# Optimization experiments

Hardware: AMD Instinct MI355X
Metric: run time of the kernel (lower is better)

Reference implementation:

```python
import jax, jax.numpy as jnp
import numpy as np

B, L, C, OUT = 8, 256, 512, 512


def setup_inputs() -> dict:
    key = jax.random.key(0)
    ks = jax.random.split(key, 8)
    xd = jax.random.normal(ks[0], (B, L, C), jnp.float32)
    xt = jax.random.normal(ks[1], (B, L, C), jnp.float32)
    # Linear weights stored (in, out): y = x @ W + b (equiv. to torch x @ W^T)
    Wc = jax.random.normal(ks[2], (C, C), jnp.float32) * 0.02
    bc = jnp.zeros((C,), jnp.float32)
    Wp = jax.random.normal(ks[3], (C, C), jnp.float32) * 0.02
    bp = jnp.zeros((C,), jnp.float32)
    Wf = jax.random.normal(ks[4], (C, OUT), jnp.float32) * 0.02
    bf = jnp.zeros((OUT,), jnp.float32)
    return {"xd": xd, "xt": xt, "Wc": Wc, "bc": bc, "Wp": Wp, "bp": bp, "Wf": Wf, "bf": bf}


def reference(xd, xt, Wc, bc, Wp, bp, Wf, bf):
    # projected features
    pt = jax.nn.relu(xt) @ Wp + bp              # (b, Lt, C)
    pc = jax.nn.relu(xd) @ Wc + bc              # (b, Ld, C)
    # sigmoid bilinear scores: (b, Lt, Ld) == (b, Ld, Lt) since Lt == Ld structurally
    scores = jax.nn.sigmoid(jnp.einsum('bic,bkc->bik', pt, pc))
    # normalize by total per-batch sum
    w = scores / jnp.sum(scores, axis=(1, 2), keepdims=True)
    # tanh of elementwise outer product, reduced with attention weights
    # cp[b,c] = sum_{i,j} tanh(xd[b,i,c] * xt[b,j,c]) * w[b,i,j]
    cp = jnp.einsum('bijc,bij->bc', jnp.tanh(xd[:, :, None, :] * xt[:, None, :, :]), w)
    return cp @ Wf + bf
```

## Files before the change

kernel.cpp:

```cpp
#include <hip/hip_runtime.h>
#include <math.h>

#define B_   8
#define L_   256
#define C_   512
#define OUT_ 512

typedef _Float16 half8 __attribute__((ext_vector_type(8)));
typedef _Float16 half4 __attribute__((ext_vector_type(4)));
typedef float    f32x4 __attribute__((ext_vector_type(4)));
typedef float    f32x2 __attribute__((ext_vector_type(2)));

__global__ __launch_bounds__(256)
void proj_mfma_kernel(const float* __restrict__ xt, const float* __restrict__ Wp,
                      const float* __restrict__ bp,
                      const float* __restrict__ xd, const float* __restrict__ Wc,
                      const float* __restrict__ bc,
                      _Float16* __restrict__ pt, _Float16* __restrict__ pc)
{
    const int which = blockIdx.z;
    const float* __restrict__ X    = which ? xd : xt;
    const float* __restrict__ W    = which ? Wc : Wp;
    const float* __restrict__ bias = which ? bc : bp;
    _Float16*    __restrict__ Y    = which ? pc : pt;

    __shared__ _Float16 Ah[2][64][40];
    __shared__ _Float16 Bh[2][64][40];
    __shared__ _Float16 Ot[64][72];

    const int tid = threadIdx.x;
    const int m0 = blockIdx.y << 6, n0 = blockIdx.x << 6;
    const int lane = tid & 63, wv = tid >> 6;
    const int l15 = lane & 15, quad = lane >> 4;

    const int srow = tid >> 2, sch = (tid & 3) << 3;
    const float* Ag = X + (size_t)(m0 + srow) * C_ + sch;
    const int nl = tid & 63, kseg = tid >> 6;
    const float* Bg = W + (size_t)(kseg << 3) * C_ + n0 + nl;

    float4 a0 = *(const float4*)(Ag);
    float4 a1 = *(const float4*)(Ag + 4);
    float wr[8];
    #pragma unroll
    for (int r = 0; r < 8; ++r) wr[r] = Bg[(size_t)r * C_];

    {
        half8 av;
        av[0] = (_Float16)fmaxf(a0.x, 0.f); av[1] = (_Float16)fmaxf(a0.y, 0.f);
        av[2] = (_Float16)fmaxf(a0.z, 0.f); av[3] = (_Float16)fmaxf(a0.w, 0.f);
        av[4] = (_Float16)fmaxf(a1.x, 0.f); av[5] = (_Float16)fmaxf(a1.y, 0.f);
        av[6] = (_Float16)fmaxf(a1.z, 0.f); av[7] = (_Float16)fmaxf(a1.w, 0.f);
        *(half8*)&Ah[0][srow][sch] = av;
        half8 bv;
        #pragma unroll
        for (int r = 0; r < 8; ++r) bv[r] = (_Float16)wr[r];
        *(half8*)&Bh[0][nl][kseg << 3] = bv;
    }

    f32x4 acc[4] = {};
    for (int ks = 0; ks < 16; ++ks) {
        const int cur = ks & 1;
        if (ks < 15) {
            Ag += 32;
            Bg += 32 * C_;
            a0 = *(const float4*)(Ag);
            a1 = *(const float4*)(Ag + 4);
            #pragma unroll
            for (int r = 0; r < 8; ++r) wr[r] = Bg[(size_t)r * C_];
        }
        __syncthreads();
        half8 af = *(const half8*)&Ah[cur][(wv << 4) + l15][quad << 3];
        #pragma unroll
        for (int nb = 0; nb < 4; ++nb) {
            half8 bf = *(const half8*)&Bh[cur][(nb << 4) + l15][quad << 3];
            acc[nb] = __builtin_amdgcn_mfma_f32_16x16x32_f16(af, bf, acc[nb], 0, 0, 0);
        }
        if (ks < 15) {
            half8 av;
            av[0] = (_Float16)fmaxf(a0.x, 0.f); av[1] = (_Float16)fmaxf(a0.y, 0.f);
            av[2] = (_Float16)fmaxf(a0.z, 0.f); av[3] = (_Float16)fmaxf(a0.w, 0.f);
            av[4] = (_Float16)fmaxf(a1.x, 0.f); av[5] = (_Float16)fmaxf(a1.y, 0.f);
            av[6] = (_Float16)fmaxf(a1.z, 0.f); av[7] = (_Float16)fmaxf(a1.w, 0.f);
            *(half8*)&Ah[cur ^ 1][srow][sch] = av;
            half8 bv;
            #pragma unroll
            for (int r = 0; r < 8; ++r) bv[r] = (_Float16)wr[r];
            *(half8*)&Bh[cur ^ 1][nl][kseg << 3] = bv;
        }
    }

    __syncthreads();
    #pragma unroll
    for (int nb = 0; nb < 4; ++nb) {
        const float bz = bias[n0 + (nb << 4) + l15];
        #pragma unroll
        for (int r = 0; r < 4; ++r)
            Ot[(wv << 4) + (quad << 2) + r][(nb << 4) + l15] = (_Float16)(acc[nb][r] + bz);
    }
    __syncthreads();
    const int erow = tid >> 3, ech = (tid & 7) << 3;
    #pragma unroll
    for (int h = 0; h < 64; h += 32)
        *(half8*)&Y[(size_t)(m0 + erow + h) * C_ + n0 + ech] = *(const half8*)&Ot[erow + h][ech];
}

__device__ __forceinline__ float sigmoid_fast(float z) {
    float e = __builtin_amdgcn_exp2f(-1.4426950408889634f * z);
    return __builtin_amdgcn_rcpf(e + 1.0f);
}

__global__ __launch_bounds__(256)
void scores_kernel(const _Float16* __restrict__ pt, const _Float16* __restrict__ pc,
                   float* __restrict__ w, float* __restrict__ sums_part)
{
    const int bx = blockIdx.x, by = blockIdx.y, b = blockIdx.z;
    const int i0 = bx << 5, j0 = by << 5;
    const int tid = threadIdx.x;
    const int lane = tid & 63, wv = tid >> 6;
    const int l15 = lane & 15, quad = lane >> 4;
    const int mq = wv >> 1, nq = wv & 1;

    __shared__ float wred[4];

    const _Float16* __restrict__ Ap =
        pt + (size_t)(b * L_ + i0 + mq * 16 + l15) * C_ + (quad << 3);
    const _Float16* __restrict__ Bp =
        pc + (size_t)(b * L_ + j0 + nq * 16 + l15) * C_ + (quad << 3);

    f32x4 acc = {};
    #pragma unroll
    for (int ks = 0; ks < 16; ++ks) {
        half8 af = *(const half8*)(Ap + (ks << 5));
        half8 bf = *(const half8*)(Bp + (ks << 5));
        acc = __builtin_amdgcn_mfma_f32_16x16x32_f16(af, bf, acc, 0, 0, 0);
    }

    float4 sg;
    sg.x = sigmoid_fast(acc[0]);
    sg.y = sigmoid_fast(acc[1]);
    sg.z = sigmoid_fast(acc[2]);
    sg.w = sigmoid_fast(acc[3]);

    float* __restrict__ wp =
        w + (size_t)(b * L_ + i0 + mq * 16 + (quad << 2)) * L_ + j0 + nq * 16 + l15;
    wp[0 * L_] = sg.x;
    wp[1 * L_] = sg.y;
    wp[2 * L_] = sg.z;
    wp[3 * L_] = sg.w;

    float lsum = (sg.x + sg.y) + (sg.z + sg.w);
    #pragma unroll
    for (int off = 32; off; off >>= 1) lsum += __shfl_xor(lsum, off);
    if (lane == 0) wred[wv] = lsum;
    __syncthreads();
    if (tid == 0)
        sums_part[(b << 6) | (bx << 3) | by] = (wred[0] + wred[1]) + (wred[2] + wred[3]);
}

__global__ __launch_bounds__(512, 8)
void tanh_cp_kernel(const float* __restrict__ w, const float* __restrict__ xd,
                    const float* __restrict__ xt, float* __restrict__ partials)
{
    const int bx = blockIdx.x, by = blockIdx.y, b = blockIdx.z;
    const int i0 = bx << 4, j0 = by << 4;
    const int tid = threadIdx.x;

    __shared__ float ws_[16][20];

    if (tid < 64) {
        const int ir = tid >> 2, j4 = (tid & 3) << 2;
        const float4 v = *(const float4*)(w + (size_t)(b * L_ + i0 + ir) * L_ + j0 + j4);
        ws_[j4 + 0][ir] = v.x;
        ws_[j4 + 1][ir] = v.y;
        ws_[j4 + 2][ir] = v.z;
        ws_[j4 + 3][ir] = v.w;
    }

    const int c = tid;
    const float* __restrict__ xdb = xd + (size_t)(b * L_ + i0) * C_ + c;
    const float* __restrict__ xtb = xt + (size_t)(b * L_ + j0) * C_ + c;

    f32x2 xds2[8];
    #pragma unroll
    for (int i = 0; i < 8; ++i) {
        xds2[i].x = xdb[(size_t)(2 * i) * C_];
        xds2[i].y = xdb[(size_t)(2 * i + 1) * C_];
    }

    __syncthreads();

    f32x2 acc01 = {0.f, 0.f}, acc23 = {0.f, 0.f};
    #pragma unroll
    for (int jj = 0; jj < 16; ++jj) {
        const float xv = xtb[(size_t)jj * C_] * 2.8853900817779268f;
        #pragma unroll
        for (int i = 0; i < 16; i += 4) {
            const float4 w4 = *(const float4*)&ws_[jj][i];
            f32x2 x01 = xds2[i >> 1] * xv;
            f32x2 e01 = { __builtin_amdgcn_exp2f(x01.x), __builtin_amdgcn_exp2f(x01.y) };
            f32x2 q01 = e01 + 1.0f;
            float rp01 = __builtin_amdgcn_rcpf(q01.x * q01.y);
            f32x2 r01 = rp01 * __builtin_shufflevector(q01, q01, 1, 0);
            f32x2 w01 = { w4.x, w4.y };
            acc01 = w01 * r01 + acc01;
            f32x2 x23 = xds2[(i >> 1) + 1] * xv;
            f32x2 e23 = { __builtin_amdgcn_exp2f(x23.x), __builtin_amdgcn_exp2f(x23.y) };
            f32x2 q23 = e23 + 1.0f;
            float rp23 = __builtin_amdgcn_rcpf(q23.x * q23.y);
            f32x2 r23 = rp23 * __builtin_shufflevector(q23, q23, 1, 0);
            f32x2 w23 = { w4.z, w4.w };
            acc23 = w23 * r23 + acc23;
        }
    }
    const int p = (bx << 4) | by;
    partials[(size_t)((b << 8) | p) * C_ + c] =
        (acc01.x + acc01.y) + (acc23.x + acc23.y);
}

__global__ __launch_bounds__(512)
void finalize_kernel(const float* __restrict__ partials, const float* __restrict__ sums_part,
                     const float* __restrict__ Wf, const float* __restrict__ bfv,
                     float* __restrict__ out)
{
    const int b = blockIdx.y;
    const int t = threadIdx.x;
    __shared__ float cp[C_];
    __shared__ float red[512];
    __shared__ float sumsh;

    red[t] = (t < 64) ? sums_part[(b << 6) | t] : 0.f;

    float s = 0.f;
    #pragma unroll 8
    for (int p = 0; p < 256; ++p)
        s += partials[(size_t)((b << 8) | p) * C_ + t];

    __syncthreads();
    for (int st = 256; st > 0; st >>= 1) {
        if (t < st) red[t] += red[t + st];
        __syncthreads();
    }
    if (t == 0) sumsh = red[0];
    __syncthreads();

    cp[t] = 1.0f - 2.0f * s / sumsh;
    __syncthreads();

    const int o  = ((int)blockIdx.x << 6) | (t & 63);
    const int c0 = (t >> 6) << 6;
    float acc = 0.f;
    #pragma unroll 8
    for (int i = 0; i < 64; ++i) {
        const int cc = c0 + i;
        acc = fmaf(cp[cc], Wf[(size_t)cc * OUT_ + o], acc);
    }
    red[t] = acc;
    __syncthreads();
    if (t < 64) {
        float a = 0.f;
        #pragma unroll
        for (int g = 0; g < 8; ++g) a += red[(g << 6) | t];
        out[(size_t)b * OUT_ + o] = a + bfv[o];
    }
}

extern "C" void kernel_launch(void* const* d_in, const int* in_sizes, int n_in,
                              void* d_out, int out_size, void* d_ws, size_t ws_size,
                              hipStream_t stream)
{
    const float* xd = (const float*)d_in[0];
    const float* xt = (const float*)d_in[1];
    const float* Wc = (const float*)d_in[2];
    const float* bc = (const float*)d_in[3];
    const float* Wp = (const float*)d_in[4];
    const float* bp = (const float*)d_in[5];
    const float* Wf = (const float*)d_in[6];
    const float* bf = (const float*)d_in[7];
    float* out = (float*)d_out;

    _Float16* pt = (_Float16*)d_ws;
    _Float16* pc = pt + 1048576;
    float* w         = (float*)(pc + 1048576);
    float* partials  = w + 524288;
    float* sums_part = partials + 1048576;

    proj_mfma_kernel<<<dim3(8, 32, 2), 256, 0, stream>>>(xt, Wp, bp, xd, Wc, bc, pt, pc);
    scores_kernel<<<dim3(8, 8, 8), 256, 0, stream>>>(pt, pc, w, sums_part);
    tanh_cp_kernel<<<dim3(16, 16, 8), 512, 0, stream>>>(w, xd, xt, partials);
    finalize_kernel<<<dim3(8, 8), 512, 0, stream>>>(partials, sums_part, Wf, bf, out);
}
```

Before: 151.6 us.

## Add fp16 prep pass, restructure projection and scores GEMMs, pipeline tanh loop

Adds a prep kernel that converts relu(x) to fp16 and transposes the weights to fp16, so the projection GEMM can read MFMA fragments straight from global memory with no LDS staging. The projection and scores kernels now give each wave one 16x16 tile with two independent accumulator chains, and the score tiles are re-shaped. The tanh kernel preloads all xt values into registers, software-pipelines its LDS weight reads across a flattened loop, changes the LDS padding and lowers the occupancy hint. This costs one extra launch and an extra global round trip for the converted data, and raises register pressure in the tanh kernel.

```diff
diff --git a/kernel.cpp b/kernel.cpp
--- a/kernel.cpp
+++ b/kernel.cpp
@@ -12,96 +12,92 @@
 typedef float    f32x2 __attribute__((ext_vector_type(2)));
 
 __global__ __launch_bounds__(256)
-void proj_mfma_kernel(const float* __restrict__ xt, const float* __restrict__ Wp,
-                      const float* __restrict__ bp,
-                      const float* __restrict__ xd, const float* __restrict__ Wc,
-                      const float* __restrict__ bc,
-                      _Float16* __restrict__ pt, _Float16* __restrict__ pc)
-{
-    const int which = blockIdx.z;
-    const float* __restrict__ X    = which ? xd : xt;
-    const float* __restrict__ W    = which ? Wc : Wp;
-    const float* __restrict__ bias = which ? bc : bp;
-    _Float16*    __restrict__ Y    = which ? pc : pt;
-
-    __shared__ _Float16 Ah[2][64][40];
-    __shared__ _Float16 Bh[2][64][40];
-    __shared__ _Float16 Ot[64][72];
-
+void prep_kernel(const float* __restrict__ xt, const float* __restrict__ xd,
+                 const float* __restrict__ Wp, const float* __restrict__ Wc,
+                 _Float16* __restrict__ Xth, _Float16* __restrict__ Xdh,
+                 _Float16* __restrict__ Wpt, _Float16* __restrict__ Wct)
+{
+    const int task = blockIdx.z;
     const int tid = threadIdx.x;
-    const int m0 = blockIdx.y << 6, n0 = blockIdx.x << 6;
-    const int lane = tid & 63, wv = tid >> 6;
-    const int l15 = lane & 15, quad = lane >> 4;
-
-    const int srow = tid >> 2, sch = (tid & 3) << 3;
-    const float* Ag = X + (size_t)(m0 + srow) * C_ + sch;
-    const int nl = tid & 63, kseg = tid >> 6;
-    const float* Bg = W + (size_t)(kseg << 3) * C_ + n0 + nl;
-
-    float4 a0 = *(const float4*)(Ag);
-    float4 a1 = *(const float4*)(Ag + 4);
-    float wr[8];
-    #pragma unroll
-    for (int r = 0; r < 8; ++r) wr[r] = Bg[(size_t)r * C_];
-
-    {
-        half8 av;
-        av[0] = (_Float16)fmaxf(a0.x, 0.f); av[1] = (_Float16)fmaxf(a0.y, 0.f);
-        av[2] = (_Float16)fmaxf(a0.z, 0.f); av[3] = (_Float16)fmaxf(a0.w, 0.f);
-        av[4] = (_Float16)fmaxf(a1.x, 0.f); av[5] = (_Float16)fmaxf(a1.y, 0.f);
-        av[6] = (_Float16)fmaxf(a1.z, 0.f); av[7] = (_Float16)fmaxf(a1.w, 0.f);
-        *(half8*)&Ah[0][srow][sch] = av;
-        half8 bv;
-        #pragma unroll
-        for (int r = 0; r < 8; ++r) bv[r] = (_Float16)wr[r];
-        *(half8*)&Bh[0][nl][kseg << 3] = bv;
-    }
-
-    f32x4 acc[4] = {};
-    for (int ks = 0; ks < 16; ++ks) {
-        const int cur = ks & 1;
-        if (ks < 15) {
-            Ag += 32;
-            Bg += 32 * C_;
-            a0 = *(const float4*)(Ag);
-            a1 = *(const float4*)(Ag + 4);
-            #pragma unroll
-            for (int r = 0; r < 8; ++r) wr[r] = Bg[(size_t)r * C_];
+    if (task < 2) {
+        const float* __restrict__ src = task ? xd : xt;
+        _Float16*    __restrict__ dst = task ? Xdh : Xth;
+        const size_t base = (size_t)blockIdx.x * 16384;
+        #pragma unroll
+        for (int it = 0; it < 16; ++it) {
+            const size_t o = base + ((size_t)it * 256 + tid) * 4;
+            const float4 v = *(const float4*)(src + o);
+            half4 h;
+            h[0] = (_Float16)fmaxf(v.x, 0.f);
+            h[1] = (_Float16)fmaxf(v.y, 0.f);
+            h[2] = (_Float16)fmaxf(v.z, 0.f);
+            h[3] = (_Float16)fmaxf(v.w, 0.f);
+            *(half4*)(dst + o) = h;
+        }
+    } else {
+        const float* __restrict__ src = (task == 3) ? Wc : Wp;
+        _Float16*    __restrict__ dst = (task == 3) ? Wct : Wpt;
+        __shared__ _Float16 tr[64][80];
+        const int tx = (blockIdx.x & 7) << 6;
+        const int ty = (blockIdx.x >> 3) << 6;
+        const int r0 = tid >> 4;
+        const int c4 = (tid & 15) << 2;
+        #pragma unroll
+        for (int p = 0; p < 4; ++p) {
+            const int kr = r0 + (p << 4);
+            const float4 v = *(const float4*)(src + (size_t)(tx + kr) * C_ + ty + c4);
+            tr[c4 + 0][kr] = (_Float16)v.x;
+            tr[c4 + 1][kr] = (_Float16)v.y;
+            tr[c4 + 2][kr] = (_Float16)v.z;
+            tr[c4 + 3][kr] = (_Float16)v.w;
         }
         __syncthreads();
-        half8 af = *(const half8*)&Ah[cur][(wv << 4) + l15][quad << 3];
-        #pragma unroll
-        for (int nb = 0; nb < 4; ++nb) {
-            half8 bf = *(const half8*)&Bh[cur][(nb << 4) + l15][quad << 3];
-            acc[nb] = __builtin_amdgcn_mfma_f32_16x16x32_f16(af, bf, acc[nb], 0, 0, 0);
-        }
-        if (ks < 15) {
-            half8 av;
-            av[0] = (_Float16)fmaxf(a0.x, 0.f); av[1] = (_Float16)fmaxf(a0.y, 0.f);
-            av[2] = (_Float16)fmaxf(a0.z, 0.f); av[3] = (_Float16)fmaxf(a0.w, 0.f);
-            av[4] = (_Float16)fmaxf(a1.x, 0.f); av[5] = (_Float16)fmaxf(a1.y, 0.f);
-            av[6] = (_Float16)fmaxf(a1.z, 0.f); av[7] = (_Float16)fmaxf(a1.w, 0.f);
-            *(half8*)&Ah[cur ^ 1][srow][sch] = av;
-            half8 bv;
-            #pragma unroll
-            for (int r = 0; r < 8; ++r) bv[r] = (_Float16)wr[r];
-            *(half8*)&Bh[cur ^ 1][nl][kseg << 3] = bv;
-        }
-    }
-
-    __syncthreads();
-    #pragma unroll
-    for (int nb = 0; nb < 4; ++nb) {
-        const float bz = bias[n0 + (nb << 4) + l15];
-        #pragma unroll
-        for (int r = 0; r < 4; ++r)
-            Ot[(wv << 4) + (quad << 2) + r][(nb << 4) + l15] = (_Float16)(acc[nb][r] + bz);
-    }
-    __syncthreads();
-    const int erow = tid >> 3, ech = (tid & 7) << 3;
-    #pragma unroll
-    for (int h = 0; h < 64; h += 32)
-        *(half8*)&Y[(size_t)(m0 + erow + h) * C_ + n0 + ech] = *(const half8*)&Ot[erow + h][ech];
+        const int nr = tid >> 3;
+        const int k8 = (tid & 7) << 3;
+        #pragma unroll
+        for (int p = 0; p < 2; ++p)
+            *(half8*)(dst + (size_t)(ty + nr + (p << 5)) * C_ + tx + k8) =
+                *(const half8*)&tr[nr + (p << 5)][k8];
+    }
+}
+
+__global__ __launch_bounds__(512)
+void proj_mfma_kernel(const _Float16* __restrict__ Xth, const _Float16* __restrict__ Xdh,
+                      const _Float16* __restrict__ Wpt, const _Float16* __restrict__ Wct,
+                      const float* __restrict__ bp, const float* __restrict__ bc,
+                      _Float16* __restrict__ pt, _Float16* __restrict__ pc)
+{
+    const int which = blockIdx.y;
+    const _Float16* __restrict__ Xh = which ? Xdh : Xth;
+    const _Float16* __restrict__ Wt = which ? Wct : Wpt;
+    const float*    __restrict__ bias = which ? bc : bp;
+    _Float16*       __restrict__ Y  = which ? pc : pt;
+
+    const int tid = threadIdx.x;
+    const int wv = tid >> 6, lane = tid & 63;
+    const int l15 = lane & 15, quad = lane >> 4;
+    const int id = ((int)blockIdx.x << 3) + wv;
+    const int m0 = (id >> 5) << 4;
+    const int n0 = (id & 31) << 4;
+
+    const _Float16* __restrict__ Ap = Xh + (size_t)(m0 + l15) * C_ + (quad << 3);
+    const _Float16* __restrict__ Bp = Wt + (size_t)(n0 + l15) * C_ + (quad << 3);
+
+    f32x4 acc0 = {}, acc1 = {};
+    #pragma unroll
+    for (int ks = 0; ks < 8; ++ks) {
+        half8 a0 = *(const half8*)(Ap + (ks << 5));
+        half8 b0 = *(const half8*)(Bp + (ks << 5));
+        acc0 = __builtin_amdgcn_mfma_f32_16x16x32_f16(a0, b0, acc0, 0, 0, 0);
+        half8 a1 = *(const half8*)(Ap + ((ks + 8) << 5));
+        half8 b1 = *(const half8*)(Bp + ((ks + 8) << 5));
+        acc1 = __builtin_amdgcn_mfma_f32_16x16x32_f16(a1, b1, acc1, 0, 0, 0);
+    }
+    const f32x4 acc = acc0 + acc1;
+    const float bz = bias[n0 + l15];
+    #pragma unroll
+    for (int r = 0; r < 4; ++r)
+        Y[(size_t)(m0 + (quad << 2) + r) * C_ + n0 + l15] = (_Float16)(acc[r] + bz);
 }
 
 __device__ __forceinline__ float sigmoid_fast(float z) {
@@ -109,31 +105,33 @@
     return __builtin_amdgcn_rcpf(e + 1.0f);
 }
 
-__global__ __launch_bounds__(256)
+__global__ __launch_bounds__(512)
 void scores_kernel(const _Float16* __restrict__ pt, const _Float16* __restrict__ pc,
                    float* __restrict__ w, float* __restrict__ sums_part)
 {
     const int bx = blockIdx.x, by = blockIdx.y, b = blockIdx.z;
-    const int i0 = bx << 5, j0 = by << 5;
     const int tid = threadIdx.x;
-    const int lane = tid & 63, wv = tid >> 6;
+    const int wv = tid >> 6, lane = tid & 63;
     const int l15 = lane & 15, quad = lane >> 4;
-    const int mq = wv >> 1, nq = wv & 1;
-
-    __shared__ float wred[4];
-
-    const _Float16* __restrict__ Ap =
-        pt + (size_t)(b * L_ + i0 + mq * 16 + l15) * C_ + (quad << 3);
-    const _Float16* __restrict__ Bp =
-        pc + (size_t)(b * L_ + j0 + nq * 16 + l15) * C_ + (quad << 3);
-
-    f32x4 acc = {};
-    #pragma unroll
-    for (int ks = 0; ks < 16; ++ks) {
-        half8 af = *(const half8*)(Ap + (ks << 5));
-        half8 bf = *(const half8*)(Bp + (ks << 5));
-        acc = __builtin_amdgcn_mfma_f32_16x16x32_f16(af, bf, acc, 0, 0, 0);
-    }
+    const int i0 = ((bx << 3) + wv) << 4;
+    const int j0 = by << 4;
+
+    __shared__ float wred[8];
+
+    const _Float16* __restrict__ Ap = pt + (size_t)(b * L_ + i0 + l15) * C_ + (quad << 3);
+    const _Float16* __restrict__ Bp = pc + (size_t)(b * L_ + j0 + l15) * C_ + (quad << 3);
+
+    f32x4 acc0 = {}, acc1 = {};
+    #pragma unroll
+    for (int ks = 0; ks < 8; ++ks) {
+        half8 a0 = *(const half8*)(Ap + (ks << 5));
+        half8 b0 = *(const half8*)(Bp + (ks << 5));
+        acc0 = __builtin_amdgcn_mfma_f32_16x16x32_f16(a0, b0, acc0, 0, 0, 0);
+        half8 a1 = *(const half8*)(Ap + ((ks + 8) << 5));
+        half8 b1 = *(const half8*)(Bp + ((ks + 8) << 5));
+        acc1 = __builtin_amdgcn_mfma_f32_16x16x32_f16(a1, b1, acc1, 0, 0, 0);
+    }
+    const f32x4 acc = acc0 + acc1;
 
     float4 sg;
     sg.x = sigmoid_fast(acc[0]);
@@ -141,8 +139,7 @@
     sg.z = sigmoid_fast(acc[2]);
     sg.w = sigmoid_fast(acc[3]);
 
-    float* __restrict__ wp =
-        w + (size_t)(b * L_ + i0 + mq * 16 + (quad << 2)) * L_ + j0 + nq * 16 + l15;
+    float* __restrict__ wp = w + (size_t)(b * L_ + i0 + (quad << 2)) * L_ + j0 + l15;
     wp[0 * L_] = sg.x;
     wp[1 * L_] = sg.y;
     wp[2 * L_] = sg.z;
@@ -153,11 +150,15 @@
     for (int off = 32; off; off >>= 1) lsum += __shfl_xor(lsum, off);
     if (lane == 0) wred[wv] = lsum;
     __syncthreads();
-    if (tid == 0)
-        sums_part[(b << 6) | (bx << 3) | by] = (wred[0] + wred[1]) + (wred[2] + wred[3]);
-}
-
-__global__ __launch_bounds__(512, 8)
+    if (tid == 0) {
+        float s = 0.f;
+        #pragma unroll
+        for (int v = 0; v < 8; ++v) s += wred[v];
+        sums_part[(b << 5) | (by << 1) | bx] = s;
+    }
+}
+
+__global__ __launch_bounds__(512, 6)
 void tanh_cp_kernel(const float* __restrict__ w, const float* __restrict__ xd,
                     const float* __restrict__ xt, float* __restrict__ partials)
 {
@@ -165,7 +166,7 @@
     const int i0 = bx << 4, j0 = by << 4;
     const int tid = threadIdx.x;
 
-    __shared__ float ws_[16][20];
+    __shared__ float ws_[16][24];
 
     if (tid < 64) {
         const int ir = tid >> 2, j4 = (tid & 3) << 2;
@@ -180,6 +181,11 @@
     const float* __restrict__ xdb = xd + (size_t)(b * L_ + i0) * C_ + c;
     const float* __restrict__ xtb = xt + (size_t)(b * L_ + j0) * C_ + c;
 
+    float xtv[16];
+    #pragma unroll
+    for (int j = 0; j < 16; ++j)
+        xtv[j] = xtb[(size_t)j * C_] * 2.8853900817779268f;
+
     f32x2 xds2[8];
     #pragma unroll
     for (int i = 0; i < 8; ++i) {
@@ -190,27 +196,32 @@
     __syncthreads();
 
     f32x2 acc01 = {0.f, 0.f}, acc23 = {0.f, 0.f};
-    #pragma unroll
-    for (int jj = 0; jj < 16; ++jj) {
-        const float xv = xtb[(size_t)jj * C_] * 2.8853900817779268f;
-        #pragma unroll
-        for (int i = 0; i < 16; i += 4) {
-            const float4 w4 = *(const float4*)&ws_[jj][i];
-            f32x2 x01 = xds2[i >> 1] * xv;
-            f32x2 e01 = { __builtin_amdgcn_exp2f(x01.x), __builtin_amdgcn_exp2f(x01.y) };
-            f32x2 q01 = e01 + 1.0f;
-            float rp01 = __builtin_amdgcn_rcpf(q01.x * q01.y);
-            f32x2 r01 = rp01 * __builtin_shufflevector(q01, q01, 1, 0);
-            f32x2 w01 = { w4.x, w4.y };
-            acc01 = w01 * r01 + acc01;
-            f32x2 x23 = xds2[(i >> 1) + 1] * xv;
-            f32x2 e23 = { __builtin_amdgcn_exp2f(x23.x), __builtin_amdgcn_exp2f(x23.y) };
-            f32x2 q23 = e23 + 1.0f;
-            float rp23 = __builtin_amdgcn_rcpf(q23.x * q23.y);
-            f32x2 r23 = rp23 * __builtin_shufflevector(q23, q23, 1, 0);
-            f32x2 w23 = { w4.z, w4.w };
-            acc23 = w23 * r23 + acc23;
+    float4 wb0 = *(const float4*)&ws_[0][0];
+    float4 wb1 = *(const float4*)&ws_[0][4];
+    #pragma unroll
+    for (int q = 0; q < 64; ++q) {
+        float4 wn = wb1;
+        if (q < 62) {
+            const int qq = q + 2;
+            wn = *(const float4*)&ws_[qq >> 2][(qq & 3) << 2];
         }
+        const float xv = xtv[q >> 2];
+        const int h = (q & 3) << 1;
+        f32x2 x01 = xds2[h] * xv;
+        f32x2 e01 = { __builtin_amdgcn_exp2f(x01.x), __builtin_amdgcn_exp2f(x01.y) };
+        f32x2 q01 = e01 + 1.0f;
+        float rp01 = __builtin_amdgcn_rcpf(q01.x * q01.y);
+        f32x2 r01 = rp01 * __builtin_shufflevector(q01, q01, 1, 0);
+        f32x2 w01 = { wb0.x, wb0.y };
+        acc01 = w01 * r01 + acc01;
+        f32x2 x23 = xds2[h + 1] * xv;
+        f32x2 e23 = { __builtin_amdgcn_exp2f(x23.x), __builtin_amdgcn_exp2f(x23.y) };
+        f32x2 q23 = e23 + 1.0f;
+        float rp23 = __builtin_amdgcn_rcpf(q23.x * q23.y);
+        f32x2 r23 = rp23 * __builtin_shufflevector(q23, q23, 1, 0);
+        f32x2 w23 = { wb0.z, wb0.w };
+        acc23 = w23 * r23 + acc23;
+        wb0 = wb1; wb1 = wn;
     }
     const int p = (bx << 4) | by;
     partials[(size_t)((b << 8) | p) * C_ + c] =
@@ -228,7 +239,7 @@
     __shared__ float red[512];
     __shared__ float sumsh;
 
-    red[t] = (t < 64) ? sums_part[(b << 6) | t] : 0.f;
+    red[t] = (t < 32) ? sums_part[(b << 5) | t] : 0.f;
 
     float s = 0.f;
     #pragma unroll 8
@@ -278,14 +289,19 @@
     const float* bf = (const float*)d_in[7];
     float* out = (float*)d_out;
 
-    _Float16* pt = (_Float16*)d_ws;
-    _Float16* pc = pt + 1048576;
+    _Float16* Xth = (_Float16*)d_ws;
+    _Float16* Xdh = Xth + 1048576;
+    _Float16* Wpt = Xdh + 1048576;
+    _Float16* Wct = Wpt + 262144;
+    _Float16* pt  = Wct + 262144;
+    _Float16* pc  = pt + 1048576;
     float* w         = (float*)(pc + 1048576);
     float* partials  = w + 524288;
     float* sums_part = partials + 1048576;
 
-    proj_mfma_kernel<<<dim3(8, 32, 2), 256, 0, stream>>>(xt, Wp, bp, xd, Wc, bc, pt, pc);
-    scores_kernel<<<dim3(8, 8, 8), 256, 0, stream>>>(pt, pc, w, sums_part);
+    prep_kernel<<<dim3(64, 1, 4), 256, 0, stream>>>(xt, xd, Wp, Wc, Xth, Xdh, Wpt, Wct);
+    proj_mfma_kernel<<<dim3(512, 2), 512, 0, stream>>>(Xth, Xdh, Wpt, Wct, bp, bc, pt, pc);
+    scores_kernel<<<dim3(2, 16, 8), 512, 0, stream>>>(pt, pc, w, sums_part);
     tanh_cp_kernel<<<dim3(16, 16, 8), 512, 0, stream>>>(w, xd, xt, partials);
     finalize_kernel<<<dim3(8, 8), 512, 0, stream>>>(partials, sums_part, Wf, bf, out);
 }
```

Result: slower. 174.3 us (+15.0%).

## Fuse all stages into one persistent kernel with grid barriers

Applied to the files above, without the earlier changes.

Replaces the four launches with a single persistent 512-block kernel that uses atomic grid barriers between phases. The phases are fp16 relu pre-conversion plus a weight transpose, the projection GEMM, a fused scores-sigmoid-tanh reduction, and the finalize. Scores no longer round-trip through global memory, and launch gaps go away. In exchange it adds a memset plus barrier spin costs, and it relies on all 512 blocks being co-resident or the barrier deadlocks.

```diff
diff --git a/kernel.cpp b/kernel.cpp
--- a/kernel.cpp
+++ b/kernel.cpp
@@ -5,262 +5,245 @@
 #define L_   256
 #define C_   512
 #define OUT_ 512
+#define NB   512
+#define NT   512
 
 typedef _Float16 half8 __attribute__((ext_vector_type(8)));
 typedef _Float16 half4 __attribute__((ext_vector_type(4)));
 typedef float    f32x4 __attribute__((ext_vector_type(4)));
 typedef float    f32x2 __attribute__((ext_vector_type(2)));
 
-__global__ __launch_bounds__(256)
-void proj_mfma_kernel(const float* __restrict__ xt, const float* __restrict__ Wp,
-                      const float* __restrict__ bp,
-                      const float* __restrict__ xd, const float* __restrict__ Wc,
-                      const float* __restrict__ bc,
-                      _Float16* __restrict__ pt, _Float16* __restrict__ pc)
-{
-    const int which = blockIdx.z;
-    const float* __restrict__ X    = which ? xd : xt;
-    const float* __restrict__ W    = which ? Wc : Wp;
-    const float* __restrict__ bias = which ? bc : bp;
-    _Float16*    __restrict__ Y    = which ? pc : pt;
-
-    __shared__ _Float16 Ah[2][64][40];
-    __shared__ _Float16 Bh[2][64][40];
-    __shared__ _Float16 Ot[64][72];
-
-    const int tid = threadIdx.x;
-    const int m0 = blockIdx.y << 6, n0 = blockIdx.x << 6;
-    const int lane = tid & 63, wv = tid >> 6;
-    const int l15 = lane & 15, quad = lane >> 4;
-
-    const int srow = tid >> 2, sch = (tid & 3) << 3;
-    const float* Ag = X + (size_t)(m0 + srow) * C_ + sch;
-    const int nl = tid & 63, kseg = tid >> 6;
-    const float* Bg = W + (size_t)(kseg << 3) * C_ + n0 + nl;
-
-    float4 a0 = *(const float4*)(Ag);
-    float4 a1 = *(const float4*)(Ag + 4);
-    float wr[8];
-    #pragma unroll
-    for (int r = 0; r < 8; ++r) wr[r] = Bg[(size_t)r * C_];
-
-    {
-        half8 av;
-        av[0] = (_Float16)fmaxf(a0.x, 0.f); av[1] = (_Float16)fmaxf(a0.y, 0.f);
-        av[2] = (_Float16)fmaxf(a0.z, 0.f); av[3] = (_Float16)fmaxf(a0.w, 0.f);
-        av[4] = (_Float16)fmaxf(a1.x, 0.f); av[5] = (_Float16)fmaxf(a1.y, 0.f);
-        av[6] = (_Float16)fmaxf(a1.z, 0.f); av[7] = (_Float16)fmaxf(a1.w, 0.f);
-        *(half8*)&Ah[0][srow][sch] = av;
-        half8 bv;
-        #pragma unroll
-        for (int r = 0; r < 8; ++r) bv[r] = (_Float16)wr[r];
-        *(half8*)&Bh[0][nl][kseg << 3] = bv;
-    }
-
-    f32x4 acc[4] = {};
-    for (int ks = 0; ks < 16; ++ks) {
-        const int cur = ks & 1;
-        if (ks < 15) {
-            Ag += 32;
-            Bg += 32 * C_;
-            a0 = *(const float4*)(Ag);
-            a1 = *(const float4*)(Ag + 4);
-            #pragma unroll
-            for (int r = 0; r < 8; ++r) wr[r] = Bg[(size_t)r * C_];
-        }
-        __syncthreads();
-        half8 af = *(const half8*)&Ah[cur][(wv << 4) + l15][quad << 3];
-        #pragma unroll
-        for (int nb = 0; nb < 4; ++nb) {
-            half8 bf = *(const half8*)&Bh[cur][(nb << 4) + l15][quad << 3];
-            acc[nb] = __builtin_amdgcn_mfma_f32_16x16x32_f16(af, bf, acc[nb], 0, 0, 0);
-        }
-        if (ks < 15) {
-            half8 av;
-            av[0] = (_Float16)fmaxf(a0.x, 0.f); av[1] = (_Float16)fmaxf(a0.y, 0.f);
-            av[2] = (_Float16)fmaxf(a0.z, 0.f); av[3] = (_Float16)fmaxf(a0.w, 0.f);
-            av[4] = (_Float16)fmaxf(a1.x, 0.f); av[5] = (_Float16)fmaxf(a1.y, 0.f);
-            av[6] = (_Float16)fmaxf(a1.z, 0.f); av[7] = (_Float16)fmaxf(a1.w, 0.f);
-            *(half8*)&Ah[cur ^ 1][srow][sch] = av;
-            half8 bv;
-            #pragma unroll
-            for (int r = 0; r < 8; ++r) bv[r] = (_Float16)wr[r];
-            *(half8*)&Bh[cur ^ 1][nl][kseg << 3] = bv;
-        }
-    }
-
-    __syncthreads();
-    #pragma unroll
-    for (int nb = 0; nb < 4; ++nb) {
-        const float bz = bias[n0 + (nb << 4) + l15];
-        #pragma unroll
-        for (int r = 0; r < 4; ++r)
-            Ot[(wv << 4) + (quad << 2) + r][(nb << 4) + l15] = (_Float16)(acc[nb][r] + bz);
-    }
-    __syncthreads();
-    const int erow = tid >> 3, ech = (tid & 7) << 3;
-    #pragma unroll
-    for (int h = 0; h < 64; h += 32)
-        *(half8*)&Y[(size_t)(m0 + erow + h) * C_ + n0 + ech] = *(const half8*)&Ot[erow + h][ech];
-}
+
+struct SmemA { _Float16 tr[64][80]; };
+struct SmemC { float red[8][256]; float ws[2][16][20]; float wred[8]; };
+struct SmemD { float cp[C_]; float redf[NT]; };
+union __align__(16) SmemU { SmemA a; SmemC c; SmemD d; };
 
 __device__ __forceinline__ float sigmoid_fast(float z) {
     float e = __builtin_amdgcn_exp2f(-1.4426950408889634f * z);
     return __builtin_amdgcn_rcpf(e + 1.0f);
 }
 
-__global__ __launch_bounds__(256)
-void scores_kernel(const _Float16* __restrict__ pt, const _Float16* __restrict__ pc,
-                   float* __restrict__ w, float* __restrict__ sums_part)
+__device__ __forceinline__ void grid_barrier(unsigned* __restrict__ bar, int k) {
+    __syncthreads();
+    if (threadIdx.x == 0) {
+        __threadfence();
+        unsigned arrived = __hip_atomic_fetch_add(&bar[k], 1u, __ATOMIC_ACQ_REL,
+                                                  __HIP_MEMORY_SCOPE_AGENT) + 1u;
+        if (arrived < (unsigned)NB) {
+            while (__hip_atomic_load(&bar[k], __ATOMIC_ACQUIRE,
+                                     __HIP_MEMORY_SCOPE_AGENT) < (unsigned)NB)
+                __builtin_amdgcn_s_sleep(8);
+        }
+    }
+    __syncthreads();
+}
+
+__global__ __launch_bounds__(NT, 4)
+void mega_kernel(const float* __restrict__ xd, const float* __restrict__ xt,
+                 const float* __restrict__ Wc, const float* __restrict__ bc,
+                 const float* __restrict__ Wp, const float* __restrict__ bp,
+                 const float* __restrict__ Wf, const float* __restrict__ bfv,
+                 unsigned* __restrict__ bar,
+                 _Float16* __restrict__ Xth, _Float16* __restrict__ Xdh,
+                 _Float16* __restrict__ Wpt, _Float16* __restrict__ Wct,
+                 _Float16* __restrict__ pt, _Float16* __restrict__ pc,
+                 float* __restrict__ cpart, float* __restrict__ tile_sum,
+                 float* __restrict__ out)
 {
-    const int bx = blockIdx.x, by = blockIdx.y, b = blockIdx.z;
-    const int i0 = bx << 5, j0 = by << 5;
-    const int tid = threadIdx.x;
-    const int lane = tid & 63, wv = tid >> 6;
-    const int l15 = lane & 15, quad = lane >> 4;
-    const int mq = wv >> 1, nq = wv & 1;
-
-    __shared__ float wred[4];
-
-    const _Float16* __restrict__ Ap =
-        pt + (size_t)(b * L_ + i0 + mq * 16 + l15) * C_ + (quad << 3);
-    const _Float16* __restrict__ Bp =
-        pc + (size_t)(b * L_ + j0 + nq * 16 + l15) * C_ + (quad << 3);
-
-    f32x4 acc = {};
-    #pragma unroll
-    for (int ks = 0; ks < 16; ++ks) {
-        half8 af = *(const half8*)(Ap + (ks << 5));
-        half8 bf = *(const half8*)(Bp + (ks << 5));
-        acc = __builtin_amdgcn_mfma_f32_16x16x32_f16(af, bf, acc, 0, 0, 0);
-    }
-
-    float4 sg;
-    sg.x = sigmoid_fast(acc[0]);
-    sg.y = sigmoid_fast(acc[1]);
-    sg.z = sigmoid_fast(acc[2]);
-    sg.w = sigmoid_fast(acc[3]);
-
-    float* __restrict__ wp =
-        w + (size_t)(b * L_ + i0 + mq * 16 + (quad << 2)) * L_ + j0 + nq * 16 + l15;
-    wp[0 * L_] = sg.x;
-    wp[1 * L_] = sg.y;
-    wp[2 * L_] = sg.z;
-    wp[3 * L_] = sg.w;
-
-    float lsum = (sg.x + sg.y) + (sg.z + sg.w);
-    #pragma unroll
-    for (int off = 32; off; off >>= 1) lsum += __shfl_xor(lsum, off);
-    if (lane == 0) wred[wv] = lsum;
-    __syncthreads();
-    if (tid == 0)
-        sums_part[(b << 6) | (bx << 3) | by] = (wred[0] + wred[1]) + (wred[2] + wred[3]);
-}
-
-__global__ __launch_bounds__(512, 8)
-void tanh_cp_kernel(const float* __restrict__ w, const float* __restrict__ xd,
-                    const float* __restrict__ xt, float* __restrict__ partials)
-{
-    const int bx = blockIdx.x, by = blockIdx.y, b = blockIdx.z;
-    const int i0 = bx << 4, j0 = by << 4;
-    const int tid = threadIdx.x;
-
-    __shared__ float ws_[16][20];
-
-    if (tid < 64) {
-        const int ir = tid >> 2, j4 = (tid & 3) << 2;
-        const float4 v = *(const float4*)(w + (size_t)(b * L_ + i0 + ir) * L_ + j0 + j4);
-        ws_[j4 + 0][ir] = v.x;
-        ws_[j4 + 1][ir] = v.y;
-        ws_[j4 + 2][ir] = v.z;
-        ws_[j4 + 3][ir] = v.w;
-    }
-
-    const int c = tid;
-    const float* __restrict__ xdb = xd + (size_t)(b * L_ + i0) * C_ + c;
-    const float* __restrict__ xtb = xt + (size_t)(b * L_ + j0) * C_ + c;
-
-    f32x2 xds2[8];
-    #pragma unroll
-    for (int i = 0; i < 8; ++i) {
-        xds2[i].x = xdb[(size_t)(2 * i) * C_];
-        xds2[i].y = xdb[(size_t)(2 * i + 1) * C_];
-    }
-
-    __syncthreads();
-
-    f32x2 acc01 = {0.f, 0.f}, acc23 = {0.f, 0.f};
-    #pragma unroll
-    for (int jj = 0; jj < 16; ++jj) {
-        const float xv = xtb[(size_t)jj * C_] * 2.8853900817779268f;
-        #pragma unroll
-        for (int i = 0; i < 16; i += 4) {
-            const float4 w4 = *(const float4*)&ws_[jj][i];
-            f32x2 x01 = xds2[i >> 1] * xv;
-            f32x2 e01 = { __builtin_amdgcn_exp2f(x01.x), __builtin_amdgcn_exp2f(x01.y) };
-            f32x2 q01 = e01 + 1.0f;
-            float rp01 = __builtin_amdgcn_rcpf(q01.x * q01.y);
-            f32x2 r01 = rp01 * __builtin_shufflevector(q01, q01, 1, 0);
-            f32x2 w01 = { w4.x, w4.y };
-            acc01 = w01 * r01 + acc01;
-            f32x2 x23 = xds2[(i >> 1) + 1] * xv;
-            f32x2 e23 = { __builtin_amdgcn_exp2f(x23.x), __builtin_amdgcn_exp2f(x23.y) };
-            f32x2 q23 = e23 + 1.0f;
-            float rp23 = __builtin_amdgcn_rcpf(q23.x * q23.y);
-            f32x2 r23 = rp23 * __builtin_shufflevector(q23, q23, 1, 0);
-            f32x2 w23 = { w4.z, w4.w };
-            acc23 = w23 * r23 + acc23;
-        }
-    }
-    const int p = (bx << 4) | by;
-    partials[(size_t)((b << 8) | p) * C_ + c] =
-        (acc01.x + acc01.y) + (acc23.x + acc23.y);
-}
-
-__global__ __launch_bounds__(512)
-void finalize_kernel(const float* __restrict__ partials, const float* __restrict__ sums_part,
-                     const float* __restrict__ Wf, const float* __restrict__ bfv,
-                     float* __restrict__ out)
-{
-    const int b = blockIdx.y;
-    const int t = threadIdx.x;
-    __shared__ float cp[C_];
-    __shared__ float red[512];
-    __shared__ float sumsh;
-
-    red[t] = (t < 64) ? sums_part[(b << 6) | t] : 0.f;
-
-    float s = 0.f;
-    #pragma unroll 8
-    for (int p = 0; p < 256; ++p)
-        s += partials[(size_t)((b << 8) | p) * C_ + t];
-
-    __syncthreads();
-    for (int st = 256; st > 0; st >>= 1) {
-        if (t < st) red[t] += red[t + st];
-        __syncthreads();
-    }
-    if (t == 0) sumsh = red[0];
-    __syncthreads();
-
-    cp[t] = 1.0f - 2.0f * s / sumsh;
-    __syncthreads();
-
-    const int o  = ((int)blockIdx.x << 6) | (t & 63);
-    const int c0 = (t >> 6) << 6;
-    float acc = 0.f;
-    #pragma unroll 8
-    for (int i = 0; i < 64; ++i) {
-        const int cc = c0 + i;
-        acc = fmaf(cp[cc], Wf[(size_t)cc * OUT_ + o], acc);
-    }
-    red[t] = acc;
-    __syncthreads();
-    if (t < 64) {
-        float a = 0.f;
-        #pragma unroll
-        for (int g = 0; g < 8; ++g) a += red[(g << 6) | t];
-        out[(size_t)b * OUT_ + o] = a + bfv[o];
+    __shared__ SmemU sm;
+    const int bid  = blockIdx.x;
+    const int tid  = threadIdx.x;
+    const int wv   = tid >> 6, lane = tid & 63;
+    const int l15  = lane & 15, quad = lane >> 4;
+
+    {
+        const int r = bid * NT + tid;
+        const float4 v1 = ((const float4*)xt)[r];
+        half4 h1;
+        h1[0] = (_Float16)fmaxf(v1.x, 0.f); h1[1] = (_Float16)fmaxf(v1.y, 0.f);
+        h1[2] = (_Float16)fmaxf(v1.z, 0.f); h1[3] = (_Float16)fmaxf(v1.w, 0.f);
+        ((half4*)Xth)[r] = h1;
+        const float4 v2 = ((const float4*)xd)[r];
+        half4 h2;
+        h2[0] = (_Float16)fmaxf(v2.x, 0.f); h2[1] = (_Float16)fmaxf(v2.y, 0.f);
+        h2[2] = (_Float16)fmaxf(v2.z, 0.f); h2[3] = (_Float16)fmaxf(v2.w, 0.f);
+        ((half4*)Xdh)[r] = h2;
+    }
+    if (bid < 128) {
+        const int which = bid >> 6, t = bid & 63;
+        const float* __restrict__ src = which ? Wc : Wp;
+        _Float16*    __restrict__ dst = which ? Wct : Wpt;
+        const int tx = (t & 7) << 6;
+        const int ty = (t >> 3) << 6;
+        const int r0 = tid >> 4;
+        const int c4 = (tid & 15) << 2;
+        #pragma unroll
+        for (int p = 0; p < 2; ++p) {
+            const int kr = r0 + (p << 5);
+            const float4 v = *(const float4*)(src + (size_t)(tx + kr) * C_ + ty + c4);
+            sm.a.tr[c4 + 0][kr] = (_Float16)v.x;
+            sm.a.tr[c4 + 1][kr] = (_Float16)v.y;
+            sm.a.tr[c4 + 2][kr] = (_Float16)v.z;
+            sm.a.tr[c4 + 3][kr] = (_Float16)v.w;
+        }
+        __syncthreads();
+        const int nr = tid >> 3, k8 = (tid & 7) << 3;
+        *(half8*)(dst + (size_t)(ty + nr) * C_ + tx + k8) = *(const half8*)&sm.a.tr[nr][k8];
+    }
+    grid_barrier(bar, 0);
+
+    {
+        const int which = bid >> 8;
+        const int r8 = bid & 255;
+        const int m0  = (r8 >> 1) << 4;
+        const int nt0 = ((r8 & 1) << 4) + wv;
+        const _Float16* __restrict__ Xh = which ? Xdh : Xth;
+        const _Float16* __restrict__ Wt = which ? Wct : Wpt;
+        const float*    __restrict__ bias = which ? bc : bp;
+        _Float16*       __restrict__ Y  = which ? pc : pt;
+        const int n0a = nt0 << 4;
+        const int n0b = (nt0 + 8) << 4;
+
+        const _Float16* __restrict__ Ap  = Xh + (size_t)(m0 + l15) * C_ + (quad << 3);
+        const _Float16* __restrict__ Bpa = Wt + (size_t)(n0a + l15) * C_ + (quad << 3);
+        const _Float16* __restrict__ Bpb = Wt + (size_t)(n0b + l15) * C_ + (quad << 3);
+        f32x4 acca = {}, accb = {};
+        #pragma unroll
+        for (int ks = 0; ks < 16; ++ks) {
+            half8 af = *(const half8*)(Ap + (ks << 5));
+            half8 ba = *(const half8*)(Bpa + (ks << 5));
+            acca = __builtin_amdgcn_mfma_f32_16x16x32_f16(af, ba, acca, 0, 0, 0);
+            half8 bb = *(const half8*)(Bpb + (ks << 5));
+            accb = __builtin_amdgcn_mfma_f32_16x16x32_f16(af, bb, accb, 0, 0, 0);
+        }
+        const float bza = bias[n0a + l15], bzb = bias[n0b + l15];
+        #pragma unroll
+        for (int r = 0; r < 4; ++r) {
+            Y[(size_t)(m0 + (quad << 2) + r) * C_ + n0a + l15] = (_Float16)(acca[r] + bza);
+            Y[(size_t)(m0 + (quad << 2) + r) * C_ + n0b + l15] = (_Float16)(accb[r] + bzb);
+        }
+    }
+    grid_barrier(bar, 1);
+
+    #pragma unroll 1
+    for (int pass = 0; pass < 2; ++pass) {
+        const int t  = bid + (pass << 9);
+        const int b  = t >> 7;
+        const int rm = t & 127;
+        const int i0 = (rm >> 3) << 4;
+        const int j0 = (rm & 7) << 5;
+
+        const float* __restrict__ xdb = xd + (size_t)(b * L_ + i0) * C_ + tid;
+        const float* __restrict__ xtb = xt + (size_t)(b * L_ + j0) * C_ + tid;
+        f32x2 xds2[8];
+        #pragma unroll
+        for (int h = 0; h < 8; ++h) {
+            xds2[h].x = xdb[(size_t)(2 * h) * C_]     * 2.8853900817779268f;
+            xds2[h].y = xdb[(size_t)(2 * h + 1) * C_] * 2.8853900817779268f;
+        }
+        float xtv[32];
+        #pragma unroll
+        for (int j = 0; j < 32; ++j) xtv[j] = xtb[(size_t)j * C_];
+
+        {
+            const int jh = wv & 1, kq = wv >> 1;
+            const _Float16* __restrict__ Ap =
+                pt + (size_t)(b * L_ + i0 + l15) * C_ + (kq << 7) + (quad << 3);
+            const _Float16* __restrict__ Bp =
+                pc + (size_t)(b * L_ + j0 + (jh << 4) + l15) * C_ + (kq << 7) + (quad << 3);
+            f32x4 acc = {};
+            #pragma unroll
+            for (int ks = 0; ks < 4; ++ks) {
+                half8 af = *(const half8*)(Ap + (ks << 5));
+                half8 bf = *(const half8*)(Bp + (ks << 5));
+                acc = __builtin_amdgcn_mfma_f32_16x16x32_f16(af, bf, acc, 0, 0, 0);
+            }
+            *(f32x4*)&sm.c.red[wv][lane << 2] = acc;
+        }
+        __syncthreads();
+        {
+            const int jh2 = tid >> 8, slot = tid & 255;
+            const float sc = (sm.c.red[jh2][slot]     + sm.c.red[jh2 + 2][slot]) +
+                             (sm.c.red[jh2 + 4][slot] + sm.c.red[jh2 + 6][slot]);
+            const float z = sigmoid_fast(sc);
+            const int ln = slot >> 2, r = slot & 3;
+            sm.c.ws[jh2][ln & 15][((ln >> 4) << 2) + r] = z;
+            float lsum = z;
+            #pragma unroll
+            for (int off = 32; off; off >>= 1) lsum += __shfl_xor(lsum, off);
+            if (lane == 0) sm.c.wred[wv] = lsum;
+        }
+        __syncthreads();
+        if (tid == 0) {
+            float ts = 0.f;
+            #pragma unroll
+            for (int v = 0; v < 8; ++v) ts += sm.c.wred[v];
+            tile_sum[t] = ts;
+        }
+
+        f32x2 acc01 = {0.f, 0.f}, acc23 = {0.f, 0.f};
+        #pragma unroll
+        for (int jh = 0; jh < 2; ++jh) {
+            #pragma unroll
+            for (int jj = 0; jj < 16; ++jj) {
+                const float xv = xtv[(jh << 4) + jj];
+                #pragma unroll
+                for (int iq = 0; iq < 4; ++iq) {
+                    const float4 w4 = *(const float4*)&sm.c.ws[jh][jj][iq << 2];
+                    f32x2 x01 = xds2[iq * 2] * xv;
+                    f32x2 e01 = { __builtin_amdgcn_exp2f(x01.x), __builtin_amdgcn_exp2f(x01.y) };
+                    f32x2 q01 = e01 + 1.0f;
+                    float rp01 = __builtin_amdgcn_rcpf(q01.x * q01.y);
+                    f32x2 r01 = rp01 * __builtin_shufflevector(q01, q01, 1, 0);
+                    f32x2 w01 = { w4.x, w4.y };
+                    acc01 = w01 * r01 + acc01;
+                    f32x2 x23 = xds2[iq * 2 + 1] * xv;
+                    f32x2 e23 = { __builtin_amdgcn_exp2f(x23.x), __builtin_amdgcn_exp2f(x23.y) };
+                    f32x2 q23 = e23 + 1.0f;
+                    float rp23 = __builtin_amdgcn_rcpf(q23.x * q23.y);
+                    f32x2 r23 = rp23 * __builtin_shufflevector(q23, q23, 1, 0);
+                    f32x2 w23 = { w4.z, w4.w };
+                    acc23 = w23 * r23 + acc23;
+                }
+            }
+        }
+        cpart[(size_t)t * C_ + tid] =
+            (acc01.x + acc01.y) + (acc23.x + acc23.y);
+    }
+    grid_barrier(bar, 2);
+
+    if (bid < 64) {
+        const int b = bid >> 3, oc = bid & 7;
+        float s = 0.f;
+        #pragma unroll 8
+        for (int rm = 0; rm < 128; ++rm)
+            s += cpart[(size_t)((b << 7) + rm) * C_ + tid];
+        if (tid < 128) sm.d.redf[tid] = tile_sum[(b << 7) + tid];
+        __syncthreads();
+        for (int st = 64; st > 0; st >>= 1) {
+            if (tid < st) sm.d.redf[tid] += sm.d.redf[tid + st];
+            __syncthreads();
+        }
+        const float S = sm.d.redf[0];
+        sm.d.cp[tid] = 1.0f - 2.0f * s / S;
+        __syncthreads();
+        const int o  = (oc << 6) | (tid & 63);
+        const int c0 = (tid >> 6) << 6;
+        float acc = 0.f;
+        #pragma unroll 8
+        for (int i = 0; i < 64; ++i) {
+            const int cc = c0 + i;
+            acc = fmaf(sm.d.cp[cc], Wf[(size_t)cc * OUT_ + o], acc);
+        }
+        sm.d.redf[tid] = acc;
+        __syncthreads();
+        if (tid < 64) {
+            float a = 0.f;
+            #pragma unroll
+            for (int g = 0; g < 8; ++g) a += sm.d.redf[(g << 6) | tid];
+            out[(size_t)b * OUT_ + ((oc << 6) | tid)] = a + bfv[(oc << 6) | tid];
+        }
     }
 }
 
@@ -268,6 +251,7 @@
                               void* d_out, int out_size, void* d_ws, size_t ws_size,
                               hipStream_t stream)
 {
+    (void)in_sizes; (void)n_in; (void)out_size; (void)ws_size;
     const float* xd = (const float*)d_in[0];
     const float* xt = (const float*)d_in[1];
     const float* Wc = (const float*)d_in[2];
@@ -278,14 +262,19 @@
     const float* bf = (const float*)d_in[7];
     float* out = (float*)d_out;
 
-    _Float16* pt = (_Float16*)d_ws;
-    _Float16* pc = pt + 1048576;
-    float* w         = (float*)(pc + 1048576);
-    float* partials  = w + 524288;
-    float* sums_part = partials + 1048576;
-
-    proj_mfma_kernel<<<dim3(8, 32, 2), 256, 0, stream>>>(xt, Wp, bp, xd, Wc, bc, pt, pc);
-    scores_kernel<<<dim3(8, 8, 8), 256, 0, stream>>>(pt, pc, w, sums_part);
-    tanh_cp_kernel<<<dim3(16, 16, 8), 512, 0, stream>>>(w, xd, xt, partials);
-    finalize_kernel<<<dim3(8, 8), 512, 0, stream>>>(partials, sums_part, Wf, bf, out);
-}
+    unsigned* bar = (unsigned*)d_ws;
+    char* p = (char*)d_ws + 4096;
+    _Float16* Xth = (_Float16*)p;            p += 2097152;
+    _Float16* Xdh = (_Float16*)p;            p += 2097152;
+    _Float16* Wpt = (_Float16*)p;            p += 524288;
+    _Float16* Wct = (_Float16*)p;            p += 524288;
+    _Float16* pt  = (_Float16*)p;            p += 2097152;
+    _Float16* pc  = (_Float16*)p;            p += 2097152;
+    float* cpart    = (float*)p;             p += 2097152;
+    float* tile_sum = (float*)p;             p += 4096;
+
+    hipMemsetAsync(d_ws, 0, 64, stream);
+    mega_kernel<<<NB, NT, 0, stream>>>(xd, xt, Wc, bc, Wp, bp, Wf, bf,
+                                       bar, Xth, Xdh, Wpt, Wct, pt, pc,
+                                       cpart, tile_sum, out);
+}
```

After: 315.6 us. 2.08x slower.
